# Kernel tuning notes

Hardware: AMD Instinct MI355X
Metric: run time of the kernel (lower is better)

## Reference

```python
import jax, jax.numpy as jnp
import numpy as np

N_NODES = 50000
N_EDGES = 800000
D = 128


def setup_inputs() -> dict:
    key = jax.random.key(0)
    ks = jax.random.split(key, 6)
    x = jax.random.normal(ks[0], (N_NODES, D), dtype=jnp.float32)
    edge_index = jax.random.randint(ks[1], (2, N_EDGES), 0, N_NODES, dtype=jnp.int32)
    scale = 1.0 / np.sqrt(D)
    W0 = jax.random.normal(ks[2], (D, D), dtype=jnp.float32) * scale
    W1 = jax.random.normal(ks[3], (D, D), dtype=jnp.float32) * scale
    W2 = jax.random.normal(ks[4], (D, D), dtype=jnp.float32) * scale
    b0 = jnp.zeros((D,), jnp.float32)
    b1 = jnp.zeros((D,), jnp.float32)
    b2 = jnp.zeros((D,), jnp.float32)
    return {"x": x, "edge_index": edge_index, "W0": W0, "b0": b0,
            "W1": W1, "b1": b1, "W2": W2, "b2": b2}


def _gcn_norm(edge_index, n_nodes, dtype):
    # symmetric normalization D^-1/2 A D^-1/2, no self loops (add_self_loops=False)
    src, dst = edge_index[1], edge_index[0]  # adj_t: aggregate src -> dst
    deg = jax.ops.segment_sum(jnp.ones(src.shape, dtype), src, num_segments=n_nodes)
    dis = jnp.where(deg > 0, jax.lax.rsqrt(jnp.maximum(deg, 1.0)), 0.0)
    return src, dst, dis[src] * dis[dst]  # per-edge norm [E]


def _gcn_layer(x, W, b, src, dst, norm, n_nodes):
    h = x @ W                                   # [N, d_out]
    msg = h[src] * norm[:, None]                # gather + scale, [E, d_out]
    agg = jax.ops.segment_sum(msg, dst, num_segments=n_nodes)
    return agg + b


def reference(x, edge_index, W0, b0, W1, b1, W2, b2):
    n = x.shape[0]
    src, dst, norm = _gcn_norm(edge_index, n, x.dtype)
    h = jax.nn.relu(_gcn_layer(x, W0, b0, src, dst, norm, n))
    h = jax.nn.relu(_gcn_layer(h, W1, b1, src, dst, norm, n))
    return _gcn_layer(h, W2, b2, src, dst, norm, n)
```

## Files before the change

kernel.cpp:

```cpp
#include <hip/hip_runtime.h>
#include <hip/hip_bf16.h>

#define DFEAT 128
#define RSPLIT 8
#define SSPLIT 64

typedef __attribute__((ext_vector_type(8))) short short8;
typedef __attribute__((ext_vector_type(4))) float f32x4;

__device__ __forceinline__ ushort f2bf(float f) {
    uint u = __float_as_uint(f);
    u += 0x7FFF + ((u >> 16) & 1);
    return (ushort)(u >> 16);
}
__device__ __forceinline__ float bf_lo(uint v) { return __uint_as_float(v << 16); }
__device__ __forceinline__ float bf_hi(uint v) { return __uint_as_float(v & 0xFFFF0000u); }


__global__ __launch_bounds__(512) void histrank_kernel(const int* __restrict__ EI,
                                                       int* __restrict__ cnt_part,
                                                       int* __restrict__ deg_part,
                                                       int* __restrict__ erank,
                                                       int nedges, int nnodes,
                                                       int range, int slice) {
    extern __shared__ int lds[];
    int* hd = lds;
    int* hs = lds + range;
    const int r = blockIdx.x & (RSPLIT - 1);
    const int s = blockIdx.x / RSPLIT;
    const int base = r * range;
    for (int i = threadIdx.x; i < 2 * range; i += 512) lds[i] = 0;
    __syncthreads();

    const int e0 = s * slice;
    const int e1 = min(nedges, e0 + slice);
    for (int e = e0 + threadIdx.x; e < e1; e += 512) {
        int dst = EI[e];
        int src = EI[nedges + e];
        unsigned ud = (unsigned)(dst - base);
        unsigned us = (unsigned)(src - base);
        if (ud < (unsigned)range) erank[e] = atomicAdd(&hd[ud], 1);
        if (us < (unsigned)range) atomicAdd(&hs[us], 1);
    }
    __syncthreads();

    for (int i = threadIdx.x; i < range; i += 512) {
        int node = base + i;
        if (node < nnodes) {
            cnt_part[s * nnodes + node] = hd[i];
            deg_part[s * nnodes + node] = hs[i];
        }
    }
}

__global__ __launch_bounds__(1024) void scan1_kernel(int* __restrict__ cnt_part,
                                                     const int* __restrict__ deg_part,
                                                     int* __restrict__ offs,
                                                     int* __restrict__ bsums,
                                                     float* __restrict__ dis, int n) {
    __shared__ int sm[1024];
    int t = threadIdx.x;
    int g = blockIdx.x * 1024 + t;
    int c = 0;
    if (g < n) {
        int d = 0;
        #pragma unroll
        for (int s = 0; s < SSPLIT; ++s) {
            int v = cnt_part[s * n + g];
            cnt_part[s * n + g] = c;
            c += v;
            d += deg_part[s * n + g];
        }
        dis[g] = (d > 0) ? rsqrtf((float)d) : 0.0f;
    }
    sm[t] = c;
    __syncthreads();
    for (int off = 1; off < 1024; off <<= 1) {
        int add = (t >= off) ? sm[t - off] : 0;
        __syncthreads();
        sm[t] += add;
        __syncthreads();
    }
    if (g < n) offs[g + 1] = sm[t];
    if (t == 1023) bsums[blockIdx.x] = sm[1023];
}

__global__ __launch_bounds__(1024) void scan3_kernel(int* __restrict__ offs,
                                                     const int* __restrict__ bsums,
                                                     int n, int nb) {
    __shared__ int pre[64];
    int t = threadIdx.x;
    if (t < 64) {
        int v = (t < nb) ? bsums[t] : 0;
        for (int off = 1; off < 64; off <<= 1) {
            int u = __shfl_up(v, off);
            if (t >= off) v += u;
        }
        int ex = __shfl_up(v, 1);
        if (t == 0) ex = 0;
        pre[t] = ex;
    }
    __syncthreads();
    int add = pre[blockIdx.x];
    int g = blockIdx.x * 1024 + t;
    if (g < n) offs[g + 1] += add;
    if (blockIdx.x == 0 && t == 0) offs[0] = 0;
}

__global__ void fill_kernel(const int* __restrict__ EI, const int* __restrict__ offs,
                            const int* __restrict__ erank, const int* __restrict__ sprefix,
                            int* __restrict__ esrc, int nedges, int nnodes, int slice) {
    int e = blockIdx.x * blockDim.x + threadIdx.x;
    if (e >= nedges) return;
    int dst = EI[e];
    int src = EI[nedges + e];
    int s = e / slice;
    int idx = offs[dst] + sprefix[s * nnodes + dst] + erank[e];
    esrc[idx] = src;
}

__global__ void prepw_kernel(const float* __restrict__ W0, const float* __restrict__ W1,
                             const float* __restrict__ W2, ushort* __restrict__ Wtb) {
    int i = blockIdx.x * 256 + threadIdx.x;
    int m = i >> 14, r = i & 16383;
    int n = r >> 7, k = r & 127;
    const float* W = (m == 0) ? W0 : (m == 1) ? W1 : W2;
    Wtb[i] = f2bf(W[k * DFEAT + n]);
}


template <int IN_F32>
__global__ __launch_bounds__(256) void gemm_mfma(const void* __restrict__ Xin,
                                                 const ushort* __restrict__ Wtb,
                                                 const float* __restrict__ dis,
                                                 ushort* __restrict__ Hb, int nrows) {
    __shared__ ushort wlds[128 * 136];
    const int t = threadIdx.x;

    #pragma unroll
    for (int q = 0; q < 8; ++q) {
        int c = t + q * 256;
        int row = c >> 4, cr = c & 15;
        short8 v = *(const short8*)(Wtb + c * 8);
        *(short8*)(&wlds[row * 136 + cr * 8]) = v;
    }

    const int lane = t & 63;
    const int r16 = lane & 15, g = lane >> 4;
    const int wv = t >> 6;
    const int rbase = blockIdx.x * 128 + wv * 16;

    short8 a[2][4];
    #pragma unroll
    for (int rt = 0; rt < 2; ++rt) {
        int row = rbase + rt * 64 + r16;
        int srow = (row < nrows) ? row : (nrows - 1);
        if (IN_F32) {
            const float* X = (const float*)Xin;
            #pragma unroll
            for (int kc = 0; kc < 4; ++kc) {
                const float* p = X + (size_t)srow * DFEAT + kc * 32 + g * 8;
                float4 f0 = *(const float4*)p;
                float4 f1 = *(const float4*)(p + 4);
                short8 sv;
                sv[0] = (short)f2bf(f0.x); sv[1] = (short)f2bf(f0.y);
                sv[2] = (short)f2bf(f0.z); sv[3] = (short)f2bf(f0.w);
                sv[4] = (short)f2bf(f1.x); sv[5] = (short)f2bf(f1.y);
                sv[6] = (short)f2bf(f1.z); sv[7] = (short)f2bf(f1.w);
                a[rt][kc] = sv;
            }
        } else {
            const ushort* X = (const ushort*)Xin;
            #pragma unroll
            for (int kc = 0; kc < 4; ++kc)
                a[rt][kc] = *(const short8*)(X + (size_t)srow * DFEAT + kc * 32 + g * 8);
        }
    }
    __syncthreads();

    f32x4 acc[2][8];
    #pragma unroll
    for (int rt = 0; rt < 2; ++rt)
        #pragma unroll
        for (int nt = 0; nt < 8; ++nt) acc[rt][nt] = (f32x4){0.f, 0.f, 0.f, 0.f};

    #pragma unroll
    for (int kc = 0; kc < 4; ++kc) {
        #pragma unroll
        for (int nt = 0; nt < 8; ++nt) {
            short8 b = *(const short8*)(&wlds[(nt * 16 + r16) * 136 + kc * 32 + g * 8]);
            acc[0][nt] = __builtin_amdgcn_mfma_f32_16x16x32_bf16(a[0][kc], b, acc[0][nt], 0, 0, 0);
            acc[1][nt] = __builtin_amdgcn_mfma_f32_16x16x32_bf16(a[1][kc], b, acc[1][nt], 0, 0, 0);
        }
    }

    #pragma unroll
    for (int rt = 0; rt < 2; ++rt) {
        const int orow_base = rbase + rt * 64 + g * 4;
        #pragma unroll
        for (int r = 0; r < 4; ++r) {
            int orow = orow_base + r;
            if (orow < nrows) {
                float d = dis[orow];
                #pragma unroll
                for (int nt = 0; nt < 8; ++nt)
                    Hb[(size_t)orow * DFEAT + nt * 16 + r16] = f2bf(acc[rt][nt][r] * d);
            }
        }
    }
}


template <int RELU, int OUT_F32>
__global__ __launch_bounds__(256) void agg_kernel(const ushort* __restrict__ H,
                                                  const int* __restrict__ offs,
                                                  const int* __restrict__ esrc,
                                                  const float* __restrict__ dis,
                                                  const float* __restrict__ bias,
                                                  void* __restrict__ OUT, int nnodes) {
    int node = blockIdx.x * 4 + (threadIdx.x >> 6);
    if (node >= nnodes) return;
    int lane = threadIdx.x & 63;
    int q = lane >> 4;
    int l16 = lane & 15;
    int s = offs[node];
    int e = offs[node + 1];

    float a0 = 0.f, a1 = 0.f, a2 = 0.f, a3 = 0.f;
    float a4 = 0.f, a5 = 0.f, a6 = 0.f, a7 = 0.f;
    float c0 = 0.f, c1 = 0.f, c2 = 0.f, c3 = 0.f;
    float c4 = 0.f, c5 = 0.f, c6 = 0.f, c7 = 0.f;
    const ushort* __restrict__ Hp = H + l16 * 8;

    int i = s + q;
    for (; i + 4 < e; i += 8) {
        int s0 = esrc[i];
        int s1 = esrc[i + 4];
        uint4 v0 = *(const uint4*)(Hp + (size_t)s0 * DFEAT);
        uint4 v1 = *(const uint4*)(Hp + (size_t)s1 * DFEAT);
        a0 += bf_lo(v0.x); a1 += bf_hi(v0.x);
        a2 += bf_lo(v0.y); a3 += bf_hi(v0.y);
        a4 += bf_lo(v0.z); a5 += bf_hi(v0.z);
        a6 += bf_lo(v0.w); a7 += bf_hi(v0.w);
        c0 += bf_lo(v1.x); c1 += bf_hi(v1.x);
        c2 += bf_lo(v1.y); c3 += bf_hi(v1.y);
        c4 += bf_lo(v1.z); c5 += bf_hi(v1.z);
        c6 += bf_lo(v1.w); c7 += bf_hi(v1.w);
    }
    if (i < e) {
        int s0 = esrc[i];
        uint4 v0 = *(const uint4*)(Hp + (size_t)s0 * DFEAT);
        a0 += bf_lo(v0.x); a1 += bf_hi(v0.x);
        a2 += bf_lo(v0.y); a3 += bf_hi(v0.y);
        a4 += bf_lo(v0.z); a5 += bf_hi(v0.z);
        a6 += bf_lo(v0.w); a7 += bf_hi(v0.w);
    }
    a0 += c0; a1 += c1; a2 += c2; a3 += c3;
    a4 += c4; a5 += c5; a6 += c6; a7 += c7;

    a0 += __shfl_xor(a0, 16); a1 += __shfl_xor(a1, 16);
    a2 += __shfl_xor(a2, 16); a3 += __shfl_xor(a3, 16);
    a4 += __shfl_xor(a4, 16); a5 += __shfl_xor(a5, 16);
    a6 += __shfl_xor(a6, 16); a7 += __shfl_xor(a7, 16);
    a0 += __shfl_xor(a0, 32); a1 += __shfl_xor(a1, 32);
    a2 += __shfl_xor(a2, 32); a3 += __shfl_xor(a3, 32);
    a4 += __shfl_xor(a4, 32); a5 += __shfl_xor(a5, 32);
    a6 += __shfl_xor(a6, 32); a7 += __shfl_xor(a7, 32);

    float dn = dis[node];
    float4 b0 = *(const float4*)&bias[l16 * 8];
    float4 b1 = *(const float4*)&bias[l16 * 8 + 4];
    float r0 = dn * a0 + b0.x, r1 = dn * a1 + b0.y;
    float r2 = dn * a2 + b0.z, r3 = dn * a3 + b0.w;
    float r4 = dn * a4 + b1.x, r5 = dn * a5 + b1.y;
    float r6 = dn * a6 + b1.z, r7 = dn * a7 + b1.w;
    if (RELU) {
        r0 = fmaxf(r0, 0.f); r1 = fmaxf(r1, 0.f);
        r2 = fmaxf(r2, 0.f); r3 = fmaxf(r3, 0.f);
        r4 = fmaxf(r4, 0.f); r5 = fmaxf(r5, 0.f);
        r6 = fmaxf(r6, 0.f); r7 = fmaxf(r7, 0.f);
    }
    if (q == 0) {
        if (OUT_F32) {
            float* o = (float*)OUT + (size_t)node * DFEAT + l16 * 8;
            *(float4*)o = make_float4(r0, r1, r2, r3);
            *(float4*)(o + 4) = make_float4(r4, r5, r6, r7);
        } else {
            uint4 p;
            p.x = (uint)f2bf(r0) | ((uint)f2bf(r1) << 16);
            p.y = (uint)f2bf(r2) | ((uint)f2bf(r3) << 16);
            p.z = (uint)f2bf(r4) | ((uint)f2bf(r5) << 16);
            p.w = (uint)f2bf(r6) | ((uint)f2bf(r7) << 16);
            *(uint4*)((ushort*)OUT + (size_t)node * DFEAT + l16 * 8) = p;
        }
    }
}


extern "C" void kernel_launch(void* const* d_in, const int* in_sizes, int n_in,
                              void* d_out, int out_size, void* d_ws, size_t ws_size,
                              hipStream_t stream) {
    const float* x  = (const float*)d_in[0];
    const int*   EI = (const int*)d_in[1];
    const float* W0 = (const float*)d_in[2];
    const float* b0 = (const float*)d_in[3];
    const float* W1 = (const float*)d_in[4];
    const float* b1 = (const float*)d_in[5];
    const float* W2 = (const float*)d_in[6];
    const float* b2 = (const float*)d_in[7];
    float* out = (float*)d_out;

    const int N = in_sizes[0] / DFEAT;
    const int E = in_sizes[1] / 2;
    const int range = (N + RSPLIT - 1) / RSPLIT;
    const int slice = (E + SSPLIT - 1) / SSPLIT;

    char* w = (char*)d_ws;
    auto alloc = [&](size_t bytes) {
        void* p = (void*)w;
        w += (bytes + 255) & ~(size_t)255;
        return p;
    };
    int*    offs  = (int*)alloc((size_t)(N + 1) * 4);
    int*    bsums = (int*)alloc(64 * 4);
    float*  dis   = (float*)alloc((size_t)N * 4);
    int*    erank = (int*)alloc((size_t)E * 4);
    int*    esrc  = (int*)alloc((size_t)E * 4);
    ushort* Wtb   = (ushort*)alloc((size_t)3 * DFEAT * DFEAT * 2);
    ushort* hbuf  = (ushort*)alloc((size_t)N * DFEAT * 2);
    ushort* abuf  = (ushort*)alloc((size_t)N * DFEAT * 2);

    int* cnt_part = (int*)hbuf;
    int* deg_part = (int*)abuf;

    const int nb = (N + 1023) / 1024;

    prepw_kernel<<<(3 * DFEAT * DFEAT) / 256, 256, 0, stream>>>(W0, W1, W2, Wtb);
    histrank_kernel<<<RSPLIT * SSPLIT, 512, 2 * range * 4, stream>>>(
        EI, cnt_part, deg_part, erank, E, N, range, slice);
    scan1_kernel<<<nb, 1024, 0, stream>>>(cnt_part, deg_part, offs, bsums, dis, N);
    scan3_kernel<<<nb, 1024, 0, stream>>>(offs, bsums, N, nb);
    fill_kernel<<<(E + 255) / 256, 256, 0, stream>>>(EI, offs, erank, cnt_part,
                                                     esrc, E, N, slice);

    const int gemmGrid = (N + 127) / 128;
    const int aggGrid  = (N + 3) / 4;

    gemm_mfma<1><<<gemmGrid, 256, 0, stream>>>(x, Wtb, dis, hbuf, N);
    agg_kernel<1, 0><<<aggGrid, 256, 0, stream>>>(hbuf, offs, esrc, dis, b0, abuf, N);
    gemm_mfma<0><<<gemmGrid, 256, 0, stream>>>(abuf, Wtb + DFEAT * DFEAT, dis, hbuf, N);
    agg_kernel<1, 0><<<aggGrid, 256, 0, stream>>>(hbuf, offs, esrc, dis, b1, abuf, N);
    gemm_mfma<0><<<gemmGrid, 256, 0, stream>>>(abuf, Wtb + 2 * DFEAT * DFEAT, dis, hbuf, N);
    agg_kernel<0, 1><<<aggGrid, 256, 0, stream>>>(hbuf, offs, esrc, dis, b2, out, N);
}
```

Before: 205.9 us.

## Split aggregation feature dimension into four passes for L2-resident gathers

The aggregation kernel is split into four feature passes of 32 columns each. Each thread now gathers 4 bytes per edge instead of 16 and accumulates two features, with a deeper unroll of four edges per iteration. The aim is to shrink the working set of gathered rows per pass so the random neighbour gathers hit cache better. In exchange, the edge indices and offsets are read four times, each gather fetches only a 64-byte slice of a row, and four times as many blocks are launched.

```diff
diff --git a/kernel.cpp b/kernel.cpp
--- a/kernel.cpp
+++ b/kernel.cpp
@@ -4,6 +4,7 @@
 #define DFEAT 128
 #define RSPLIT 8
 #define SSPLIT 64
+#define FPASS 4
 
 typedef __attribute__((ext_vector_type(8))) short short8;
 typedef __attribute__((ext_vector_type(4))) float f32x4;
@@ -217,81 +218,60 @@
                                                   const int* __restrict__ esrc,
                                                   const float* __restrict__ dis,
                                                   const float* __restrict__ bias,
-                                                  void* __restrict__ OUT, int nnodes) {
-    int node = blockIdx.x * 4 + (threadIdx.x >> 6);
+                                                  void* __restrict__ OUT,
+                                                  int nnodes, int bpp) {
+    int pass = blockIdx.x / bpp;
+    int node = (blockIdx.x - pass * bpp) * 4 + (threadIdx.x >> 6);
     if (node >= nnodes) return;
     int lane = threadIdx.x & 63;
     int q = lane >> 4;
     int l16 = lane & 15;
     int s = offs[node];
     int e = offs[node + 1];
-
-    float a0 = 0.f, a1 = 0.f, a2 = 0.f, a3 = 0.f;
-    float a4 = 0.f, a5 = 0.f, a6 = 0.f, a7 = 0.f;
-    float c0 = 0.f, c1 = 0.f, c2 = 0.f, c3 = 0.f;
-    float c4 = 0.f, c5 = 0.f, c6 = 0.f, c7 = 0.f;
-    const ushort* __restrict__ Hp = H + l16 * 8;
+    int fb = pass * 32 + l16 * 2;
+
+    const ushort* __restrict__ Hp = H + fb;
+
+    float a0 = 0.f, a1 = 0.f, b0_ = 0.f, b1_ = 0.f;
+    float c0 = 0.f, c1 = 0.f, d0 = 0.f, d1 = 0.f;
 
     int i = s + q;
-    for (; i + 4 < e; i += 8) {
+    for (; i + 12 < e; i += 16) {
         int s0 = esrc[i];
         int s1 = esrc[i + 4];
-        uint4 v0 = *(const uint4*)(Hp + (size_t)s0 * DFEAT);
-        uint4 v1 = *(const uint4*)(Hp + (size_t)s1 * DFEAT);
-        a0 += bf_lo(v0.x); a1 += bf_hi(v0.x);
-        a2 += bf_lo(v0.y); a3 += bf_hi(v0.y);
-        a4 += bf_lo(v0.z); a5 += bf_hi(v0.z);
-        a6 += bf_lo(v0.w); a7 += bf_hi(v0.w);
-        c0 += bf_lo(v1.x); c1 += bf_hi(v1.x);
-        c2 += bf_lo(v1.y); c3 += bf_hi(v1.y);
-        c4 += bf_lo(v1.z); c5 += bf_hi(v1.z);
-        c6 += bf_lo(v1.w); c7 += bf_hi(v1.w);
-    }
-    if (i < e) {
+        int s2 = esrc[i + 8];
+        int s3 = esrc[i + 12];
+        uint v0 = *(const uint*)(Hp + (size_t)s0 * DFEAT);
+        uint v1 = *(const uint*)(Hp + (size_t)s1 * DFEAT);
+        uint v2 = *(const uint*)(Hp + (size_t)s2 * DFEAT);
+        uint v3 = *(const uint*)(Hp + (size_t)s3 * DFEAT);
+        a0 += bf_lo(v0); a1 += bf_hi(v0);
+        b0_ += bf_lo(v1); b1_ += bf_hi(v1);
+        c0 += bf_lo(v2); c1 += bf_hi(v2);
+        d0 += bf_lo(v3); d1 += bf_hi(v3);
+    }
+    for (; i < e; i += 4) {
         int s0 = esrc[i];
-        uint4 v0 = *(const uint4*)(Hp + (size_t)s0 * DFEAT);
-        a0 += bf_lo(v0.x); a1 += bf_hi(v0.x);
-        a2 += bf_lo(v0.y); a3 += bf_hi(v0.y);
-        a4 += bf_lo(v0.z); a5 += bf_hi(v0.z);
-        a6 += bf_lo(v0.w); a7 += bf_hi(v0.w);
-    }
-    a0 += c0; a1 += c1; a2 += c2; a3 += c3;
-    a4 += c4; a5 += c5; a6 += c6; a7 += c7;
+        uint v0 = *(const uint*)(Hp + (size_t)s0 * DFEAT);
+        a0 += bf_lo(v0); a1 += bf_hi(v0);
+    }
+    a0 += b0_ + c0 + d0;
+    a1 += b1_ + c1 + d1;
 
     a0 += __shfl_xor(a0, 16); a1 += __shfl_xor(a1, 16);
-    a2 += __shfl_xor(a2, 16); a3 += __shfl_xor(a3, 16);
-    a4 += __shfl_xor(a4, 16); a5 += __shfl_xor(a5, 16);
-    a6 += __shfl_xor(a6, 16); a7 += __shfl_xor(a7, 16);
     a0 += __shfl_xor(a0, 32); a1 += __shfl_xor(a1, 32);
-    a2 += __shfl_xor(a2, 32); a3 += __shfl_xor(a3, 32);
-    a4 += __shfl_xor(a4, 32); a5 += __shfl_xor(a5, 32);
-    a6 += __shfl_xor(a6, 32); a7 += __shfl_xor(a7, 32);
 
     float dn = dis[node];
-    float4 b0 = *(const float4*)&bias[l16 * 8];
-    float4 b1 = *(const float4*)&bias[l16 * 8 + 4];
-    float r0 = dn * a0 + b0.x, r1 = dn * a1 + b0.y;
-    float r2 = dn * a2 + b0.z, r3 = dn * a3 + b0.w;
-    float r4 = dn * a4 + b1.x, r5 = dn * a5 + b1.y;
-    float r6 = dn * a6 + b1.z, r7 = dn * a7 + b1.w;
-    if (RELU) {
-        r0 = fmaxf(r0, 0.f); r1 = fmaxf(r1, 0.f);
-        r2 = fmaxf(r2, 0.f); r3 = fmaxf(r3, 0.f);
-        r4 = fmaxf(r4, 0.f); r5 = fmaxf(r5, 0.f);
-        r6 = fmaxf(r6, 0.f); r7 = fmaxf(r7, 0.f);
-    }
+    float2 bb = *(const float2*)&bias[fb];
+    float r0 = dn * a0 + bb.x;
+    float r1 = dn * a1 + bb.y;
+    if (RELU) { r0 = fmaxf(r0, 0.f); r1 = fmaxf(r1, 0.f); }
     if (q == 0) {
         if (OUT_F32) {
-            float* o = (float*)OUT + (size_t)node * DFEAT + l16 * 8;
-            *(float4*)o = make_float4(r0, r1, r2, r3);
-            *(float4*)(o + 4) = make_float4(r4, r5, r6, r7);
+            *(float2*)((float*)OUT + (size_t)node * DFEAT + fb) = make_float2(r0, r1);
         } else {
-            uint4 p;
-            p.x = (uint)f2bf(r0) | ((uint)f2bf(r1) << 16);
-            p.y = (uint)f2bf(r2) | ((uint)f2bf(r3) << 16);
-            p.z = (uint)f2bf(r4) | ((uint)f2bf(r5) << 16);
-            p.w = (uint)f2bf(r6) | ((uint)f2bf(r7) << 16);
-            *(uint4*)((ushort*)OUT + (size_t)node * DFEAT + l16 * 8) = p;
+            uint p = (uint)f2bf(r0) | ((uint)f2bf(r1) << 16);
+            *(uint*)((ushort*)OUT + (size_t)node * DFEAT + fb) = p;
         }
     }
 }
@@ -344,12 +324,13 @@
                                                      esrc, E, N, slice);
 
     const int gemmGrid = (N + 127) / 128;
-    const int aggGrid  = (N + 3) / 4;
+    const int bpp      = (N + 3) / 4;
+    const int aggGrid  = bpp * FPASS;
 
     gemm_mfma<1><<<gemmGrid, 256, 0, stream>>>(x, Wtb, dis, hbuf, N);
-    agg_kernel<1, 0><<<aggGrid, 256, 0, stream>>>(hbuf, offs, esrc, dis, b0, abuf, N);
+    agg_kernel<1, 0><<<aggGrid, 256, 0, stream>>>(hbuf, offs, esrc, dis, b0, abuf, N, bpp);
     gemm_mfma<0><<<gemmGrid, 256, 0, stream>>>(abuf, Wtb + DFEAT * DFEAT, dis, hbuf, N);
-    agg_kernel<1, 0><<<aggGrid, 256, 0, stream>>>(hbuf, offs, esrc, dis, b1, abuf, N);
+    agg_kernel<1, 0><<<aggGrid, 256, 0, stream>>>(hbuf, offs, esrc, dis, b1, abuf, N, bpp);
     gemm_mfma<0><<<gemmGrid, 256, 0, stream>>>(abuf, Wtb + 2 * DFEAT * DFEAT, dis, hbuf, N);
-    agg_kernel<0, 1><<<aggGrid, 256, 0, stream>>>(hbuf, offs, esrc, dis, b2, out, N);
-}
+    agg_kernel<0, 1><<<aggGrid, 256, 0, stream>>>(hbuf, offs, esrc, dis, b2, out, N, bpp);
+}
```

After: 372.7 us. +81.0%, slower.
